# Performance work log

Hardware: AMD Instinct MI355X
Metric: run time of the kernel (lower is better)

Reference implementation:

```python
import jax, jax.numpy as jnp
import numpy as np


def setup_inputs() -> dict:
    key = jax.random.key(0)
    k1, k2 = jax.random.split(key)
    B, C, M, N = 4, 3, 4096, 8192
    query = jax.random.normal(k1, (B, C, M), dtype=jnp.float32)
    points = jax.random.normal(k2, (B, C, N), dtype=jnp.float32)
    return {"k": 16, "query": query, "points": points}


def reference(k, query, points):
    # query: BxCxM, points: BxCxN  (trans=True path of original module)
    q = jnp.swapaxes(query, 1, 2)   # BxMxC
    p = jnp.swapaxes(points, 1, 2)  # BxNxC
    # squared L2 distances (FAISS GpuIndexFlatL2): BxMxN
    q2 = jnp.sum(q * q, axis=-1, keepdims=True)           # BxMx1
    p2 = jnp.sum(p * p, axis=-1)[:, None, :]              # Bx1xN
    dist = q2 + p2 - 2.0 * jnp.einsum('bmc,bnc->bmn', q, p)
    # k smallest distances, sorted ascending (FAISS sorts results)
    _, index_batch = jax.lax.top_k(-dist, k)              # BxMxK int32
    index_batch = index_batch.astype(jnp.int64) if index_batch.dtype != jnp.int64 else index_batch
    # gather neighbor coordinates: points BxCxN, idx BxMxK -> BxCxMxK
    neighbor_points = jax.vmap(lambda pts, idx: pts[:, idx])(points, index_batch)
    return neighbor_points, index_batch
```

## Files before the change

### kernel.cpp

```cpp
#include <hip/hip_runtime.h>
#include <stdint.h>

#define BQ 4
#define CC 3
#define MM 4096
#define NN 8192
#define KK 16
#define NP_OFF (BQ*CC*MM*KK)
#define BLOCK 512
#define RPW 8
#define GROUPS 2
#define QTS 4
#define ROWS (GROUPS*RPW)
#define CHUNK 1024
#define NCH (NN/CHUNK)
#define CST (CHUNK/64)
#define QST (CST/QTS)
#define EPSD 1e-4f

__device__ __forceinline__ float rfl(float x) {
    return __uint_as_float((unsigned)__builtin_amdgcn_readfirstlane((int)__float_as_uint(x)));
}
__device__ __forceinline__ unsigned mapf(float f) {
    unsigned u = __float_as_uint(f);
    return (u & 0x80000000u) ? ~u : (u | 0x80000000u);
}
__device__ __forceinline__ float unmapf(unsigned u) {
    unsigned b = (u & 0x80000000u) ? (u & 0x7fffffffu) : ~u;
    return __uint_as_float(b);
}

__global__ __launch_bounds__(BLOCK, 8) void knn_kernel(
    const float* __restrict__ query,
    const float* __restrict__ points,
    float* __restrict__ out)
{
    __shared__ float4 pts[2][CHUNK];
    __shared__ unsigned aux[ROWS][64];
    __shared__ unsigned scnt[ROWS];
    __shared__ unsigned rcbits[ROWS];

    const int tid  = threadIdx.x;
    const int lane = tid & 63;
    const int wv   = tid >> 6;
    const int g    = wv >> 2;
    const int qt   = wv & 3;
    const int bid  = blockIdx.x;
    const int b    = bid >> 8;
    const int rb   = (bid & 255) * ROWS;

    const float* pb = points + b * (CC * NN);
    const float* qb = query  + b * (CC * MM);

    ((unsigned*)aux)[tid]       = 0u;
    ((unsigned*)aux)[tid + 512] = 0u;
    if (tid < ROWS) scnt[tid] = 0u;

    float qx[RPW], qy[RPW], qz[RPW], dm[RPW];
    #pragma unroll
    for (int r = 0; r < RPW; ++r) {
        int m = rb + g * RPW + r;
        qx[r] = rfl(qb[m]);
        qy[r] = rfl(qb[MM + m]);
        qz[r] = rfl(qb[2*MM + m]);
        dm[r] = -__builtin_inff();
    }

    auto stage = [&](int ch, int bi) {
        #pragma unroll
        for (int i = 0; i < CHUNK / BLOCK; ++i) {
            int ii = i * BLOCK + tid;
            int n  = ch * CHUNK + ii;
            float px = pb[n], py = pb[NN + n], pz = pb[2*NN + n];
            float p2 = __fadd_rn(__fadd_rn(__fmul_rn(px,px), __fmul_rn(py,py)),
                                 __fmul_rn(pz,pz));
            pts[bi][ii] = make_float4(px, py, pz, -0.5f * p2);
        }
    };

    auto comp1 = [&](int bi) {
        #pragma unroll
        for (int t = 0; t < QST; ++t) {
            float4 P = pts[bi][((qt * QST + t) << 6) + lane];
            #pragma unroll
            for (int r = 0; r < RPW; ++r) {
                float dotf = __builtin_fmaf(qz[r], P.z,
                              __builtin_fmaf(qy[r], P.y,
                               __builtin_fmaf(qx[r], P.x, P.w)));
                dm[r] = fmaxf(dm[r], dotf);
            }
        }
    };

    stage(0, 0);
    #pragma unroll 1
    for (int ch = 0; ch < NCH; ch += 2) {
        __syncthreads();
        if (ch + 1 < NCH) stage(ch + 1, 1);
        comp1(0);
        __syncthreads();
        if (ch + 2 < NCH) stage(ch + 2, 0);
        if (ch + 1 < NCH) comp1(1);
    }

    #pragma unroll
    for (int r = 0; r < RPW; ++r)
        atomicMax(&aux[g*RPW + r][lane], mapf(dm[r]));
    __syncthreads();

    #pragma unroll
    for (int rr = 0; rr < 2; ++rr) {
        int row = 2*wv + rr;
        unsigned v = aux[row][lane];
        #pragma unroll
        for (int k = 2; k <= 64; k <<= 1) {
            #pragma unroll
            for (int j = k >> 1; j > 0; j >>= 1) {
                unsigned o = __shfl_xor(v, j, 64);
                bool keepmin = (((lane & j) == 0) == ((lane & k) == 0));
                v = keepmin ? (v < o ? v : o) : (v > o ? v : o);
            }
        }
        unsigned tb = __shfl(v, 48, 64);
        if (lane == 0) rcbits[row] = __float_as_uint(unmapf(tb) - EPSD);
    }
    __syncthreads();

    float rc[RPW];
    #pragma unroll
    for (int r = 0; r < RPW; ++r)
        rc[r] = rfl(__uint_as_float(rcbits[g*RPW + r]));

    auto comp2 = [&](int ch, int bi) {
        #pragma unroll
        for (int t = 0; t < QST; ++t) {
            int st = qt * QST + t;
            float4 P = pts[bi][(st << 6) + lane];
            unsigned n = (unsigned)(ch * CHUNK + (st << 6) + lane);
            #pragma unroll
            for (int r = 0; r < RPW; ++r) {
                float dotf = __builtin_fmaf(qz[r], P.z,
                              __builtin_fmaf(qy[r], P.y,
                               __builtin_fmaf(qx[r], P.x, P.w)));
                if (dotf >= rc[r]) {
                    unsigned pos = atomicAdd(&scnt[g*RPW + r], 1u);
                    if (pos < 64u) aux[g*RPW + r][pos] = n;
                }
            }
        }
    };

    stage(0, 0);
    #pragma unroll 1
    for (int ch = 0; ch < NCH; ch += 2) {
        __syncthreads();
        if (ch + 1 < NCH) stage(ch + 1, 1);
        comp2(ch, 0);
        __syncthreads();
        if (ch + 2 < NCH) stage(ch + 2, 0);
        if (ch + 1 < NCH) comp2(ch + 1, 1);
    }
    __syncthreads();

    #pragma unroll
    for (int rr = 0; rr < 2; ++rr) {
        int row = 2*wv + rr;
        int m   = rb + row;
        float ex = rfl(qb[m]);
        float ey = rfl(qb[MM + m]);
        float ez = rfl(qb[2*MM + m]);
        float eq2 = rfl(__fadd_rn(__fadd_rn(__fmul_rn(ex,ex), __fmul_rn(ey,ey)),
                                  __fmul_rn(ez,ez)));
        unsigned c = scnt[row]; if (c > 64u) c = 64u;
        unsigned kb = 0xffffffffu, id = 0xffffffffu;
        if (lane < (int)c) {
            id = aux[row][lane];
            float px = pb[id], py = pb[NN + id], pz = pb[2*NN + id];
            float p2 = __fadd_rn(__fadd_rn(__fmul_rn(px,px), __fmul_rn(py,py)),
                                 __fmul_rn(pz,pz));
            float dot = __builtin_fmaf(ez, pz,
                         __builtin_fmaf(ey, py, __fmul_rn(ex, px)));
            float d = __fsub_rn(__fadd_rn(eq2, p2), __fmul_rn(2.0f, dot));
            unsigned fb = __float_as_uint(d);
            kb = (fb & 0x80000000u) ? ~fb : (fb | 0x80000000u);
        }
        #pragma unroll
        for (int k = 2; k <= 64; k <<= 1) {
            #pragma unroll
            for (int j = k >> 1; j > 0; j >>= 1) {
                unsigned ok = __shfl_xor(kb, j, 64);
                unsigned oi = __shfl_xor(id, j, 64);
                bool takeMin  = (((lane & j) == 0) == ((lane & k) == 0));
                bool selfLess = (kb < ok) || (kb == ok && id < oi);
                if (selfLess != takeMin) { kb = ok; id = oi; }
            }
        }
        if (lane < KK) {
            int oi = (int)id;
            out[NP_OFF + (b * MM + m) * KK + lane] = (float)oi;
            out[((b * CC + 0) * MM + m) * KK + lane] = pb[oi];
            out[((b * CC + 1) * MM + m) * KK + lane] = pb[NN + oi];
            out[((b * CC + 2) * MM + m) * KK + lane] = pb[2*NN + oi];
        }
    }
}

extern "C" void kernel_launch(void* const* d_in, const int* in_sizes, int n_in,
                              void* d_out, int out_size, void* d_ws, size_t ws_size,
                              hipStream_t stream) {
    const float* query  = (const float*)d_in[1];
    const float* points = (const float*)d_in[2];
    float* out = (float*)d_out;
    dim3 grid(BQ * (MM / ROWS));
    dim3 block(BLOCK);
    knn_kernel<<<grid, block, 0, stream>>>(query, points, out);
}
```

Before: 105.5 us.

## Precompute packed point float4 in prep kernel and register-prefetch chunks

Adds a small prep kernel that packs each point as (x,y,z,-0.5*|p|^2) into the workspace, so the main kernel no longer reloads strided SoA coordinates and recomputes norms in every block. The chunk staging is restructured into a register prefetch: the next chunk's float4s are loaded into registers while the current buffer is computed, with one barrier per chunk instead of two. The second pass reuses the last chunk left in shared memory (chunk 7, then 6) and reorders chunk processing to avoid a reload. The cost is an extra kernel launch, workspace traffic, and more live registers for the prefetched values.

```diff
diff --git a/kernel.cpp b/kernel.cpp
--- a/kernel.cpp
+++ b/kernel.cpp
@@ -10,12 +10,10 @@
 #define BLOCK 512
 #define RPW 8
 #define GROUPS 2
-#define QTS 4
-#define ROWS (GROUPS*RPW)
+#define ROWS 16
 #define CHUNK 1024
 #define NCH (NN/CHUNK)
-#define CST (CHUNK/64)
-#define QST (CST/QTS)
+#define QST 4
 #define EPSD 1e-4f
 
 __device__ __forceinline__ float rfl(float x) {
@@ -30,9 +28,22 @@
     return __uint_as_float(b);
 }
 
+__global__ __launch_bounds__(256) void prep_kernel(
+    const float* __restrict__ points, float4* __restrict__ ws4)
+{
+    int i = blockIdx.x * 256 + threadIdx.x;
+    int b = i >> 13, n = i & (NN - 1);
+    const float* pb = points + b * (CC * NN);
+    float px = pb[n], py = pb[NN + n], pz = pb[2*NN + n];
+    float p2 = __fadd_rn(__fadd_rn(__fmul_rn(px,px), __fmul_rn(py,py)),
+                         __fmul_rn(pz,pz));
+    ws4[i] = make_float4(px, py, pz, -0.5f * p2);
+}
+
 __global__ __launch_bounds__(BLOCK, 8) void knn_kernel(
     const float* __restrict__ query,
     const float* __restrict__ points,
+    const float4* __restrict__ ws4,
     float* __restrict__ out)
 {
     __shared__ float4 pts[2][CHUNK];
@@ -49,8 +60,9 @@
     const int b    = bid >> 8;
     const int rb   = (bid & 255) * ROWS;
 
-    const float* pb = points + b * (CC * NN);
-    const float* qb = query  + b * (CC * MM);
+    const float*  pb  = points + b * (CC * NN);
+    const float*  qb  = query  + b * (CC * MM);
+    const float4* wsb = ws4 + b * NN;
 
     ((unsigned*)aux)[tid]       = 0u;
     ((unsigned*)aux)[tid + 512] = 0u;
@@ -66,16 +78,14 @@
         dm[r] = -__builtin_inff();
     }
 
-    auto stage = [&](int ch, int bi) {
-        #pragma unroll
-        for (int i = 0; i < CHUNK / BLOCK; ++i) {
-            int ii = i * BLOCK + tid;
-            int n  = ch * CHUNK + ii;
-            float px = pb[n], py = pb[NN + n], pz = pb[2*NN + n];
-            float p2 = __fadd_rn(__fadd_rn(__fmul_rn(px,px), __fmul_rn(py,py)),
-                                 __fmul_rn(pz,pz));
-            pts[bi][ii] = make_float4(px, py, pz, -0.5f * p2);
-        }
+    float4 pre0, pre1;
+    auto loadc = [&](int ch) {
+        pre0 = wsb[(ch << 10) + tid];
+        pre1 = wsb[(ch << 10) + 512 + tid];
+    };
+    auto writec = [&](int bi) {
+        pts[bi][tid]       = pre0;
+        pts[bi][512 + tid] = pre1;
     };
 
     auto comp1 = [&](int bi) {
@@ -92,20 +102,21 @@
         }
     };
 
-    stage(0, 0);
+    loadc(0);
     #pragma unroll 1
-    for (int ch = 0; ch < NCH; ch += 2) {
+    for (int ch = 0; ch < NCH; ++ch) {
+        int bi = ch & 1;
+        writec(bi);
+        if (ch + 1 < NCH) loadc(ch + 1);
+        if (ch > 0) comp1(bi ^ 1);
         __syncthreads();
-        if (ch + 1 < NCH) stage(ch + 1, 1);
-        comp1(0);
-        __syncthreads();
-        if (ch + 2 < NCH) stage(ch + 2, 0);
-        if (ch + 1 < NCH) comp1(1);
-    }
+    }
+    comp1(1);
 
     #pragma unroll
     for (int r = 0; r < RPW; ++r)
         atomicMax(&aux[g*RPW + r][lane], mapf(dm[r]));
+    loadc(0);
     __syncthreads();
 
     #pragma unroll
@@ -136,7 +147,7 @@
         for (int t = 0; t < QST; ++t) {
             int st = qt * QST + t;
             float4 P = pts[bi][(st << 6) + lane];
-            unsigned n = (unsigned)(ch * CHUNK + (st << 6) + lane);
+            unsigned n = (unsigned)((ch << 10) + (st << 6) + lane);
             #pragma unroll
             for (int r = 0; r < RPW; ++r) {
                 float dotf = __builtin_fmaf(qz[r], P.z,
@@ -150,16 +161,17 @@
         }
     };
 
-    stage(0, 0);
+    comp2(6, 0);
+    __syncthreads();
     #pragma unroll 1
-    for (int ch = 0; ch < NCH; ch += 2) {
+    for (int i = 0; i < 6; ++i) {
+        writec(i & 1);
+        if (i < 5) loadc(i + 1);
+        int c = (i == 0) ? 7 : (i - 1);
+        comp2(c, c & 1);
         __syncthreads();
-        if (ch + 1 < NCH) stage(ch + 1, 1);
-        comp2(ch, 0);
-        __syncthreads();
-        if (ch + 2 < NCH) stage(ch + 2, 0);
-        if (ch + 1 < NCH) comp2(ch + 1, 1);
-    }
+    }
+    comp2(5, 1);
     __syncthreads();
 
     #pragma unroll
@@ -181,8 +193,7 @@
             float dot = __builtin_fmaf(ez, pz,
                          __builtin_fmaf(ey, py, __fmul_rn(ex, px)));
             float d = __fsub_rn(__fadd_rn(eq2, p2), __fmul_rn(2.0f, dot));
-            unsigned fb = __float_as_uint(d);
-            kb = (fb & 0x80000000u) ? ~fb : (fb | 0x80000000u);
+            kb = mapf(d);
         }
         #pragma unroll
         for (int k = 2; k <= 64; k <<= 1) {
@@ -210,8 +221,10 @@
                               hipStream_t stream) {
     const float* query  = (const float*)d_in[1];
     const float* points = (const float*)d_in[2];
+    float4* ws4 = (float4*)d_ws;
     float* out = (float*)d_out;
+    prep_kernel<<<dim3((BQ*NN)/256), dim3(256), 0, stream>>>(points, ws4);
     dim3 grid(BQ * (MM / ROWS));
     dim3 block(BLOCK);
-    knn_kernel<<<grid, block, 0, stream>>>(query, points, out);
-}
+    knn_kernel<<<grid, block, 0, stream>>>(query, points, ws4, out);
+}
```

New measurement: 106.5 us. Within noise of the previous version (+0.9%).
